# Kernel tuning notes

Hardware: AMD Instinct MI355X
Metric: run time of the kernel (lower is better)

The kernel has to match this reference:

```python
import jax, jax.numpy as jnp
import numpy as np

HIDDEN = 1024
N_HEADS = 16
HEAD_DIM = HIDDEN // N_HEADS  # 64


def setup_inputs() -> dict:
    key = jax.random.key(0)
    k1, k2, k3 = jax.random.split(key, 3)
    x = jax.random.normal(k1, (2, 2048, HIDDEN), dtype=jnp.float32)
    # nn.Linear(hidden, 3*hidden, bias=False): weight [3*hidden, hidden]
    w_qkv = jax.random.normal(k2, (3 * HIDDEN, HIDDEN), dtype=jnp.float32) * (HIDDEN ** -0.5)
    # nn.Linear(hidden, hidden, bias=False): weight [hidden, hidden]
    w_dense = jax.random.normal(k3, (HIDDEN, HIDDEN), dtype=jnp.float32) * (HIDDEN ** -0.5)
    return {"x": x, "w_qkv": w_qkv, "w_dense": w_dense}


def reference(x, w_qkv, w_dense):
    B, S, D = x.shape
    # Fused QKV projection: y = x @ w_qkv.T -> [B, S, 3*D]
    qkv = jnp.einsum("bsd,ed->bse", x, w_qkv)
    q, k, v = jnp.split(qkv, 3, axis=-1)

    def heads(t):  # [B,S,D] -> [B,H,S,hd]
        return t.reshape(B, S, N_HEADS, HEAD_DIM).transpose(0, 2, 1, 3)

    q, k, v = heads(q), heads(k), heads(v)
    scale = jnp.asarray(HEAD_DIM, x.dtype) ** -0.5
    scores = jnp.einsum("bhqd,bhkd->bhqk", q, k) * scale  # [B,H,S,S]
    probs = jax.nn.softmax(scores, axis=-1)
    ctx = jnp.einsum("bhqk,bhkd->bhqd", probs, v)  # [B,H,S,hd]
    ctx = ctx.transpose(0, 2, 1, 3).reshape(B, S, D)
    # Output dense: ctx @ w_dense.T
    return jnp.einsum("bsd,ed->bse", ctx, w_dense)
```

## Files before the change

kernel.cpp:

```cpp
#include <hip/hip_runtime.h>

typedef unsigned short u16;
typedef unsigned int u32;
typedef __bf16 bf16x8 __attribute__((ext_vector_type(8)));
typedef float f32x4 __attribute__((ext_vector_type(4)));
typedef u16 u16x8 __attribute__((ext_vector_type(8)));
typedef u16 u16x4 __attribute__((ext_vector_type(4)));
typedef u32 u32x2 __attribute__((ext_vector_type(2)));

__device__ __forceinline__ u16 to_bf16(float f) {
  unsigned int u = __builtin_bit_cast(unsigned int, f);
  u += 0x7fffu + ((u >> 16) & 1u);
  return (u16)(u >> 16);
}

__device__ __forceinline__ f32x4 mfma16(bf16x8 a, bf16x8 b, f32x4 c) {
  return __builtin_amdgcn_mfma_f32_16x16x32_bf16(a, b, c, 0, 0, 0);
}

#define GLD16(gp, lp) __builtin_amdgcn_global_load_lds( \
    (const __attribute__((address_space(1))) unsigned int*)(gp), \
    (__attribute__((address_space(3))) unsigned int*)(lp), 16, 0, 0)

#define WAITVM(N) asm volatile("s_waitcnt vmcnt(" #N ")" ::: "memory")
#define BARRIER() asm volatile("s_barrier" ::: "memory")

__global__ __launch_bounds__(256) void cvt_all(
    const float* __restrict__ x, const float* __restrict__ wq, const float* __restrict__ wd,
    u16* __restrict__ xb, u16* __restrict__ wqb, u16* __restrict__ wdb) {
  long i = ((long)blockIdx.x * 256 + threadIdx.x) * 4;
  const float* s; u16* d;
  if (i < 4194304)      { s = x  + i;             d = xb  + i; }
  else if (i < 7340032) { s = wq + (i - 4194304); d = wqb + (i - 4194304); }
  else                  { s = wd + (i - 7340032); d = wdb + (i - 7340032); }
  f32x4 f = *(const f32x4*)s;
  u16x4 o;
  o[0] = to_bf16(f[0]); o[1] = to_bf16(f[1]); o[2] = to_bf16(f[2]); o[3] = to_bf16(f[3]);
  *(u16x4*)d = o;
}

__global__ __launch_bounds__(256) void gemm_qkv(const u16* __restrict__ A,
    const u16* __restrict__ Bt, u16* __restrict__ qk, u16* __restrict__ vt,
    int K, float qscale) {
  __shared__ __align__(16) u16 As[2][4096];
  __shared__ __align__(16) u16 Bs[2][4096];
  const int tid = threadIdx.x;
  const int lane = tid & 63, wave = tid >> 6;
  const int wm = (wave & 1) * 64, wn = (wave >> 1) * 64;
  const int bm = blockIdx.y * 128, bn = blockIdx.x * 128;
  const int fm = lane & 15, fk8 = (lane >> 4) * 8;
  f32x4 acc[4][4] = {};

  const int r0 = tid >> 2, c0 = (tid & 3) * 8;
  const u16* Ag = A + (long)(bm + r0) * K + c0;
  const u16* Bg = Bt + (long)(bn + r0) * K + c0;
  const long rowStep = (long)64 * K;

#define GSTAGE(K0, IB) do { \
    GLD16(Ag + (K0),           &As[IB][tid * 8]); \
    GLD16(Ag + rowStep + (K0), &As[IB][tid * 8 + 2048]); \
    GLD16(Bg + (K0),           &Bs[IB][tid * 8]); \
    GLD16(Bg + rowStep + (K0), &Bs[IB][tid * 8 + 2048]); \
  } while (0)

  GSTAGE(0, 0);
  int ib = 0;
  for (int k0 = 0; k0 < K; k0 += 32) {
    if (k0 + 32 < K) { GSTAGE(k0 + 32, ib ^ 1); WAITVM(4); }
    else             { WAITVM(0); }
    BARRIER();
    bf16x8 a[4], b[4];
#pragma unroll
    for (int i = 0; i < 4; i++) a[i] = *(const bf16x8*)&As[ib][(wm + i * 16 + fm) * 32 + fk8];
#pragma unroll
    for (int j = 0; j < 4; j++) b[j] = *(const bf16x8*)&Bs[ib][(wn + j * 16 + fm) * 32 + fk8];
#pragma unroll
    for (int i = 0; i < 4; i++)
#pragma unroll
      for (int j = 0; j < 4; j++)
        acc[i][j] = mfma16(a[i], b[j], acc[i][j]);
    BARRIER();
    ib ^= 1;
  }
#undef GSTAGE

  const int er = (lane >> 4) * 4, ec = lane & 15;
  if (bn >= 2048) {
#pragma unroll
    for (int i = 0; i < 4; i++) {
      const long row0 = bm + wm + i * 16 + er;
      const long bb = row0 >> 11;
      const int kv = (int)(row0 & 2047);
#pragma unroll
      for (int j = 0; j < 4; j++) {
        const int dcol = bn + wn + j * 16 + ec - 2048;
        u16x4 pk;
#pragma unroll
        for (int r = 0; r < 4; r++) pk[r] = to_bf16(acc[i][j][r]);
        *(u16x4*)&vt[((bb * 16 + (dcol >> 6)) * 64 + (dcol & 63)) * 2048 + kv] = pk;
      }
    }
  } else {
    const float sc = (bn < 1024) ? qscale : 1.0f;
#pragma unroll
    for (int i = 0; i < 4; i++)
#pragma unroll
      for (int j = 0; j < 4; j++)
#pragma unroll
        for (int r = 0; r < 4; r++) {
          long row = bm + wm + i * 16 + er + r;
          long col = bn + wn + j * 16 + ec;
          qk[row * 2048 + col] = to_bf16(acc[i][j][r] * sc);
        }
  }
}

__global__ __launch_bounds__(256) void gemm_bt_n64(const u16* __restrict__ A,
    const u16* __restrict__ Bt, float* __restrict__ C, int M, int N, int K) {
  __shared__ __align__(16) u16 As[2][4096];
  __shared__ __align__(16) u16 Bs[2][2048];
  const int tid = threadIdx.x;
  const int lane = tid & 63, wave = tid >> 6;
  const int wm = (wave & 1) * 64, wn = (wave >> 1) * 32;
  const int bm = blockIdx.y * 128, bn = blockIdx.x * 64;
  const int fm = lane & 15, fk8 = (lane >> 4) * 8;
  f32x4 acc[4][2] = {};

  const int r0 = tid >> 2, c0 = (tid & 3) * 8;
  const u16* Ag = A + (long)(bm + r0) * K + c0;
  const u16* Bg = Bt + (long)(bn + r0) * K + c0;
  const long rowStep = (long)64 * K;

#define GSTAGE(K0, IB) do { \
    GLD16(Ag + (K0),           &As[IB][tid * 8]); \
    GLD16(Ag + rowStep + (K0), &As[IB][tid * 8 + 2048]); \
    GLD16(Bg + (K0),           &Bs[IB][tid * 8]); \
  } while (0)

  GSTAGE(0, 0);
  int ib = 0;
  for (int k0 = 0; k0 < K; k0 += 32) {
    if (k0 + 32 < K) { GSTAGE(k0 + 32, ib ^ 1); WAITVM(3); }
    else             { WAITVM(0); }
    BARRIER();
    bf16x8 a[4], b[2];
#pragma unroll
    for (int i = 0; i < 4; i++) a[i] = *(const bf16x8*)&As[ib][(wm + i * 16 + fm) * 32 + fk8];
#pragma unroll
    for (int j = 0; j < 2; j++) b[j] = *(const bf16x8*)&Bs[ib][(wn + j * 16 + fm) * 32 + fk8];
#pragma unroll
    for (int i = 0; i < 4; i++)
#pragma unroll
      for (int j = 0; j < 2; j++)
        acc[i][j] = mfma16(a[i], b[j], acc[i][j]);
    BARRIER();
    ib ^= 1;
  }
#undef GSTAGE

  const int er = (lane >> 4) * 4, ec = lane & 15;
#pragma unroll
  for (int i = 0; i < 4; i++)
#pragma unroll
    for (int j = 0; j < 2; j++)
#pragma unroll
      for (int r = 0; r < 4; r++)
        C[(long)(bm + wm + i * 16 + er + r) * N + bn + wn + j * 16 + ec] = acc[i][j][r];
}

__global__ __launch_bounds__(256) void attn_kernel(const u16* __restrict__ qk,
                                                   const u16* __restrict__ vt,
                                                   u16* __restrict__ ctx) {
  __shared__ __align__(16) u16 Kb[2][4096];
  __shared__ __align__(16) u16 Vb[2][4096];
  __shared__ __align__(16) u16 Ps[128 * 64];
  const int tid = threadIdx.x, lane = tid & 63, wave = tid >> 6;
  const int fm = lane & 15, g = lane >> 4, f7 = fm & 7;

  const int id = blockIdx.x;
  const int c = id & 7, m = id >> 3;
  const int qt = m & 15, bh = (m >> 4) * 8 + c;
  const int b = bh >> 4, h = bh & 15;
  const long tokBase = (long)b * 2048;
  const int q0 = qt * 128;

  const int sr8 = lane >> 3;
  const int gch = (lane & 7) ^ sr8;
  const u16* Kg = qk + (tokBase + wave * 16 + sr8) * 2048 + 1024 + h * 64 + gch * 8;
  const u16* Vg = vt + ((long)bh * 64 + wave * 16 + sr8) * 2048 + gch * 8;
  u16* KL = &Kb[0][wave * 16 * 64] + lane * 8;
  u16* VL = &Vb[0][wave * 16 * 64] + lane * 8;

#define STAGE(S0, IB) do { \
    GLD16(Kg + (long)(S0) * 2048,          KL + (IB) * 4096); \
    GLD16(Kg + (long)((S0) + 8) * 2048,    KL + (IB) * 4096 + 512); \
    GLD16(Vg + (S0),                       VL + (IB) * 4096); \
    GLD16(Vg + (S0) + (long)8 * 2048,      VL + (IB) * 4096 + 512); \
  } while (0)

  STAGE(0, 0);

  bf16x8 qa[2][2];
#pragma unroll
  for (int t = 0; t < 2; t++) {
    const long qoff = (tokBase + q0 + wave * 32 + t * 16 + fm) * 2048 + h * 64;
    qa[t][0] = *(const bf16x8*)&qk[qoff + g * 8];
    qa[t][1] = *(const bf16x8*)&qk[qoff + 32 + g * 8];
  }

  f32x4 o[2][4] = {};
  f32x4 ol[2] = {};
  u16x8 onesu = {0x3F80, 0x3F80, 0x3F80, 0x3F80, 0x3F80, 0x3F80, 0x3F80, 0x3F80};
  bf16x8 ones = __builtin_bit_cast(bf16x8, onesu);

  int ib = 0;
  for (int s0 = 0; s0 < 2048; s0 += 64) {
    if (s0 + 64 < 2048) { STAGE(s0 + 64, ib ^ 1); WAITVM(4); }
    else                { WAITVM(0); }
    BARRIER();

    const u16* Kt = &Kb[ib][0];
    const u16* Vtile = &Vb[ib][0];

#pragma unroll
    for (int jj = 0; jj < 4; jj++) {
      bf16x8 k0 = *(const bf16x8*)&Kt[(jj * 16 + fm) * 64 + ((g    ) ^ f7) * 8];
      bf16x8 k1 = *(const bf16x8*)&Kt[(jj * 16 + fm) * 64 + ((4 + g) ^ f7) * 8];
#pragma unroll
      for (int t = 0; t < 2; t++) {
        f32x4 s = {};
        s = mfma16(k0, qa[t][0], s);
        s = mfma16(k1, qa[t][1], s);
        u32 p0r = __builtin_bit_cast(u32, __builtin_amdgcn_exp2f(s[0])) + 0x8000u;
        u32 p1r = __builtin_bit_cast(u32, __builtin_amdgcn_exp2f(s[1])) + 0x8000u;
        u32 p2r = __builtin_bit_cast(u32, __builtin_amdgcn_exp2f(s[2])) + 0x8000u;
        u32 p3r = __builtin_bit_cast(u32, __builtin_amdgcn_exp2f(s[3])) + 0x8000u;
        u32x2 wv;
        wv[0] = __builtin_amdgcn_perm(p1r, p0r, 0x07060302u);
        wv[1] = __builtin_amdgcn_perm(p3r, p2r, 0x07060302u);
        const int slot = (jj * 4 + g) ^ (2 * f7);
        *(u32x2*)((u32*)&Ps[(wave * 32 + t * 16 + fm) * 64] + slot * 2) = wv;
      }
    }

#pragma unroll
    for (int ks = 0; ks < 2; ks++) {
      bf16x8 vb[4];
#pragma unroll
      for (int jd = 0; jd < 4; jd++)
        vb[jd] = *(const bf16x8*)&Vtile[(jd * 16 + fm) * 64 + ((ks * 4 + g) ^ f7) * 8];
#pragma unroll
      for (int t = 0; t < 2; t++) {
        bf16x8 pa = *(const bf16x8*)&Ps[(wave * 32 + t * 16 + fm) * 64 +
                                        ((4 * ks + g) ^ f7) * 8];
#pragma unroll
        for (int jd = 0; jd < 4; jd++)
          o[t][jd] = mfma16(pa, vb[jd], o[t][jd]);
        ol[t] = mfma16(pa, ones, ol[t]);
      }
    }
    BARRIER();
    ib ^= 1;
  }
#undef STAGE

#pragma unroll
  for (int t = 0; t < 2; t++) {
#pragma unroll
    for (int r = 0; r < 4; r++) {
      float inv = 1.0f / ol[t][r];
      const long obase = (tokBase + q0 + wave * 32 + t * 16 + g * 4 + r) * 1024 + h * 64;
#pragma unroll
      for (int jd = 0; jd < 4; jd++)
        ctx[obase + jd * 16 + fm] = to_bf16(o[t][jd][r] * inv);
    }
  }
}

extern "C" void kernel_launch(void* const* d_in, const int* in_sizes, int n_in,
                              void* d_out, int out_size, void* d_ws, size_t ws_size,
                              hipStream_t stream) {
  const float* x  = (const float*)d_in[0];
  const float* wq = (const float*)d_in[1];
  const float* wd = (const float*)d_in[2];
  float* out = (float*)d_out;
  char* ws = (char*)d_ws;
  u16* xb   = (u16*)(ws);
  u16* wqb  = (u16*)(ws + 8388608);
  u16* wdb  = (u16*)(ws + 14680064);
  u16* qkb  = (u16*)(ws + 16777216);
  u16* vtb  = (u16*)(ws + 33554432);
  u16* ctxb = (u16*)(ws + 41943040);

  const float sscale = 0.125f * 1.44269504f;

  cvt_all<<<8192, 256, 0, stream>>>(x, wq, wd, xb, wqb, wdb);
  gemm_qkv<<<dim3(24, 32), 256, 0, stream>>>(xb, wqb, qkb, vtb, 1024, sscale);
  attn_kernel<<<512, 256, 0, stream>>>(qkb, vtb, ctxb);
  gemm_bt_n64<<<dim3(16, 32), 256, 0, stream>>>(ctxb, wdb, out, 4096, 1024, 1024);
}
```

Before: 180.2 us.

## Split attention KV tile across 8 waves with register-resident P and cross-wave reduction

Attention blocks now use 512 threads. Each of the 8 waves handles 64 queries against a 16-key slice of each 64-key tile, instead of 32 queries against all keys. The probabilities stay in registers as operands for the 16x16x16 bf16 MFMA (packed with v_cvt_pk_bf16_f32), which removes the LDS round-trip for the P matrix. Partial O and row-sum accumulators are merged across the four KV-slice waves through shared memory at the end, and s_setprio is raised around the PV MFMAs. The trade-off is extra reduction barriers, more accumulator registers per wave, and use of the narrower-K MFMA for PV.

```diff
diff --git a/kernel.cpp b/kernel.cpp
--- a/kernel.cpp
+++ b/kernel.cpp
@@ -6,6 +6,7 @@
 typedef float f32x4 __attribute__((ext_vector_type(4)));
 typedef u16 u16x8 __attribute__((ext_vector_type(8)));
 typedef u16 u16x4 __attribute__((ext_vector_type(4)));
+typedef short s16x4 __attribute__((ext_vector_type(4)));
 typedef u32 u32x2 __attribute__((ext_vector_type(2)));
 
 __device__ __forceinline__ u16 to_bf16(float f) {
@@ -16,6 +17,14 @@
 
 __device__ __forceinline__ f32x4 mfma16(bf16x8 a, bf16x8 b, f32x4 c) {
   return __builtin_amdgcn_mfma_f32_16x16x32_bf16(a, b, c, 0, 0, 0);
+}
+
+__device__ __forceinline__ f32x4 mfma1k(s16x4 a, s16x4 b, f32x4 c) {
+  return __builtin_amdgcn_mfma_f32_16x16x16bf16_1k(a, b, c, 0, 0, 0);
+}
+
+__device__ __forceinline__ u32 cvtpk(float a, float b) {
+  u32 r; asm("v_cvt_pk_bf16_f32 %0, %1, %2" : "=v"(r) : "v"(a), "v"(b)); return r;
 }
 
 #define GLD16(gp, lp) __builtin_amdgcn_global_load_lds( \
@@ -168,14 +177,14 @@
         C[(long)(bm + wm + i * 16 + er + r) * N + bn + wn + j * 16 + ec] = acc[i][j][r];
 }
 
-__global__ __launch_bounds__(256) void attn_kernel(const u16* __restrict__ qk,
+__global__ __launch_bounds__(512) void attn_kernel(const u16* __restrict__ qk,
                                                    const u16* __restrict__ vt,
                                                    u16* __restrict__ ctx) {
-  __shared__ __align__(16) u16 Kb[2][4096];
-  __shared__ __align__(16) u16 Vb[2][4096];
-  __shared__ __align__(16) u16 Ps[128 * 64];
+  __shared__ __align__(16) u16 smem[16384];
+  __shared__ __align__(16) float lred[8][64];
   const int tid = threadIdx.x, lane = tid & 63, wave = tid >> 6;
   const int fm = lane & 15, g = lane >> 4, f7 = fm & 7;
+  const int qh = wave & 1, kvq = wave >> 1;
 
   const int id = blockIdx.x;
   const int c = id & 7, m = id >> 3;
@@ -186,93 +195,120 @@
 
   const int sr8 = lane >> 3;
   const int gch = (lane & 7) ^ sr8;
-  const u16* Kg = qk + (tokBase + wave * 16 + sr8) * 2048 + 1024 + h * 64 + gch * 8;
-  const u16* Vg = vt + ((long)bh * 64 + wave * 16 + sr8) * 2048 + gch * 8;
-  u16* KL = &Kb[0][wave * 16 * 64] + lane * 8;
-  u16* VL = &Vb[0][wave * 16 * 64] + lane * 8;
+  const u16* Kg = qk + (tokBase + wave * 8 + sr8) * 2048 + 1024 + h * 64 + gch * 8;
+  const u16* Vg = vt + ((long)bh * 64 + wave * 8 + sr8) * 2048 + gch * 8;
+  u16* KL = &smem[wave * 512] + lane * 8;
+  u16* VL = &smem[8192 + wave * 512] + lane * 8;
 
 #define STAGE(S0, IB) do { \
-    GLD16(Kg + (long)(S0) * 2048,          KL + (IB) * 4096); \
-    GLD16(Kg + (long)((S0) + 8) * 2048,    KL + (IB) * 4096 + 512); \
-    GLD16(Vg + (S0),                       VL + (IB) * 4096); \
-    GLD16(Vg + (S0) + (long)8 * 2048,      VL + (IB) * 4096 + 512); \
+    GLD16(Kg + (long)(S0) * 2048, KL + (IB) * 4096); \
+    GLD16(Vg + (S0),              VL + (IB) * 4096); \
   } while (0)
 
   STAGE(0, 0);
 
-  bf16x8 qa[2][2];
-#pragma unroll
-  for (int t = 0; t < 2; t++) {
-    const long qoff = (tokBase + q0 + wave * 32 + t * 16 + fm) * 2048 + h * 64;
-    qa[t][0] = *(const bf16x8*)&qk[qoff + g * 8];
-    qa[t][1] = *(const bf16x8*)&qk[qoff + 32 + g * 8];
-  }
-
-  f32x4 o[2][4] = {};
-  f32x4 ol[2] = {};
-  u16x8 onesu = {0x3F80, 0x3F80, 0x3F80, 0x3F80, 0x3F80, 0x3F80, 0x3F80, 0x3F80};
-  bf16x8 ones = __builtin_bit_cast(bf16x8, onesu);
+  bf16x8 qa[4][2];
+#pragma unroll
+  for (int qb = 0; qb < 4; qb++) {
+    const long qoff = (tokBase + q0 + qh * 64 + qb * 16 + fm) * 2048 + h * 64;
+    qa[qb][0] = *(const bf16x8*)&qk[qoff + g * 8];
+    qa[qb][1] = *(const bf16x8*)&qk[qoff + 32 + g * 8];
+  }
+
+  f32x4 o[4][4] = {};
+  f32x4 ol[4] = {};
+  const s16x4 onesb = {0x3F80, 0x3F80, 0x3F80, 0x3F80};
 
   int ib = 0;
   for (int s0 = 0; s0 < 2048; s0 += 64) {
-    if (s0 + 64 < 2048) { STAGE(s0 + 64, ib ^ 1); WAITVM(4); }
+    if (s0 + 64 < 2048) { STAGE(s0 + 64, ib ^ 1); WAITVM(2); }
     else                { WAITVM(0); }
     BARRIER();
-
-    const u16* Kt = &Kb[ib][0];
-    const u16* Vtile = &Vb[ib][0];
-
-#pragma unroll
-    for (int jj = 0; jj < 4; jj++) {
-      bf16x8 k0 = *(const bf16x8*)&Kt[(jj * 16 + fm) * 64 + ((g    ) ^ f7) * 8];
-      bf16x8 k1 = *(const bf16x8*)&Kt[(jj * 16 + fm) * 64 + ((4 + g) ^ f7) * 8];
-#pragma unroll
-      for (int t = 0; t < 2; t++) {
-        f32x4 s = {};
-        s = mfma16(k0, qa[t][0], s);
-        s = mfma16(k1, qa[t][1], s);
-        u32 p0r = __builtin_bit_cast(u32, __builtin_amdgcn_exp2f(s[0])) + 0x8000u;
-        u32 p1r = __builtin_bit_cast(u32, __builtin_amdgcn_exp2f(s[1])) + 0x8000u;
-        u32 p2r = __builtin_bit_cast(u32, __builtin_amdgcn_exp2f(s[2])) + 0x8000u;
-        u32 p3r = __builtin_bit_cast(u32, __builtin_amdgcn_exp2f(s[3])) + 0x8000u;
-        u32x2 wv;
-        wv[0] = __builtin_amdgcn_perm(p1r, p0r, 0x07060302u);
-        wv[1] = __builtin_amdgcn_perm(p3r, p2r, 0x07060302u);
-        const int slot = (jj * 4 + g) ^ (2 * f7);
-        *(u32x2*)((u32*)&Ps[(wave * 32 + t * 16 + fm) * 64] + slot * 2) = wv;
-      }
+    const u16* Kt = &smem[ib * 4096];
+    const u16* Vt = &smem[8192 + ib * 4096];
+
+    bf16x8 ka0 = *(const bf16x8*)&Kt[(kvq * 16 + fm) * 64 + ((g) ^ f7) * 8];
+    bf16x8 ka1 = *(const bf16x8*)&Kt[(kvq * 16 + fm) * 64 + ((4 + g) ^ f7) * 8];
+    u16x4 vbu[4];
+#pragma unroll
+    for (int db = 0; db < 4; db++)
+      vbu[db] = *(const u16x4*)&Vt[(db * 16 + fm) * 64 +
+                                   ((kvq * 2 + (g >> 1)) ^ f7) * 8 + (g & 1) * 4];
+
+    s16x4 pa[4];
+#pragma unroll
+    for (int qb = 0; qb < 4; qb++) {
+      f32x4 s = {};
+      s = mfma16(ka0, qa[qb][0], s);
+      s = mfma16(ka1, qa[qb][1], s);
+      u32x2 pk;
+      pk[0] = cvtpk(__builtin_amdgcn_exp2f(s[0]), __builtin_amdgcn_exp2f(s[1]));
+      pk[1] = cvtpk(__builtin_amdgcn_exp2f(s[2]), __builtin_amdgcn_exp2f(s[3]));
+      pa[qb] = __builtin_bit_cast(s16x4, pk);
     }
 
-#pragma unroll
-    for (int ks = 0; ks < 2; ks++) {
-      bf16x8 vb[4];
-#pragma unroll
-      for (int jd = 0; jd < 4; jd++)
-        vb[jd] = *(const bf16x8*)&Vtile[(jd * 16 + fm) * 64 + ((ks * 4 + g) ^ f7) * 8];
-#pragma unroll
-      for (int t = 0; t < 2; t++) {
-        bf16x8 pa = *(const bf16x8*)&Ps[(wave * 32 + t * 16 + fm) * 64 +
-                                        ((4 * ks + g) ^ f7) * 8];
-#pragma unroll
-        for (int jd = 0; jd < 4; jd++)
-          o[t][jd] = mfma16(pa, vb[jd], o[t][jd]);
-        ol[t] = mfma16(pa, ones, ol[t]);
-      }
+    __builtin_amdgcn_s_setprio(1);
+#pragma unroll
+    for (int qb = 0; qb < 4; qb++) {
+#pragma unroll
+      for (int db = 0; db < 4; db++)
+        o[qb][db] = mfma1k(pa[qb], __builtin_bit_cast(s16x4, vbu[db]), o[qb][db]);
+      ol[qb] = mfma1k(pa[qb], onesb, ol[qb]);
     }
+    __builtin_amdgcn_s_setprio(0);
     BARRIER();
     ib ^= 1;
   }
 #undef STAGE
 
-#pragma unroll
-  for (int t = 0; t < 2; t++) {
-#pragma unroll
-    for (int r = 0; r < 4; r++) {
-      float inv = 1.0f / ol[t][r];
-      const long obase = (tokBase + q0 + wave * 32 + t * 16 + g * 4 + r) * 1024 + h * 64;
-#pragma unroll
-      for (int jd = 0; jd < 4; jd++)
-        ctx[obase + jd * 16 + fm] = to_bf16(o[t][jd][r] * inv);
+  __syncthreads();
+  float* red = (float*)&smem[0];
+
+#define WR_O(SLOT) do { \
+    _Pragma("unroll") for (int qb = 0; qb < 4; qb++) { \
+      _Pragma("unroll") for (int db = 0; db < 4; db++) \
+        *(f32x4*)&red[(SLOT) * 4096 + (qb * 4 + db) * 256 + lane * 4] = o[qb][db]; \
+      if (fm == 0) *(f32x4*)&lred[wave][qb * 16 + g * 4] = ol[qb]; \
+    } \
+  } while (0)
+
+#define RD_O(SLOT, PW) do { \
+    _Pragma("unroll") for (int qb = 0; qb < 4; qb++) { \
+      _Pragma("unroll") for (int db = 0; db < 4; db++) { \
+        f32x4 t = *(const f32x4*)&red[(SLOT) * 4096 + (qb * 4 + db) * 256 + lane * 4]; \
+        o[qb][db] += t; \
+      } \
+      f32x4 lt = *(const f32x4*)&lred[PW][qb * 16 + g * 4]; \
+      ol[qb] += lt; \
+    } \
+  } while (0)
+
+  if (wave == 4 || wave == 5) WR_O(wave - 4);
+  __syncthreads();
+  if (wave == 0 || wave == 1) RD_O(wave, wave + 4);
+  __syncthreads();
+  if (wave == 6 || wave == 7) WR_O(wave - 6);
+  __syncthreads();
+  if (wave == 2 || wave == 3) RD_O(wave - 2, wave + 4);
+  __syncthreads();
+  if (wave == 2 || wave == 3) WR_O(wave - 2);
+  __syncthreads();
+  if (wave == 0 || wave == 1) RD_O(wave, wave + 2);
+#undef WR_O
+#undef RD_O
+
+  if (wave < 2) {
+#pragma unroll
+    for (int qb = 0; qb < 4; qb++) {
+      f32x4 inv;
+#pragma unroll
+      for (int r = 0; r < 4; r++) inv[r] = 1.0f / ol[qb][r];
+#pragma unroll
+      for (int db = 0; db < 4; db++)
+#pragma unroll
+        for (int r = 0; r < 4; r++)
+          ctx[(tokBase + q0 + qh * 64 + qb * 16 + g * 4 + r) * 1024 + h * 64 + db * 16 + fm] =
+              to_bf16(o[qb][db][r] * inv[r]);
     }
   }
 }
@@ -296,6 +332,6 @@
 
   cvt_all<<<8192, 256, 0, stream>>>(x, wq, wd, xb, wqb, wdb);
   gemm_qkv<<<dim3(24, 32), 256, 0, stream>>>(xb, wqb, qkb, vtb, 1024, sscale);
-  attn_kernel<<<512, 256, 0, stream>>>(qkb, vtb, ctxb);
+  attn_kernel<<<512, 512, 0, stream>>>(qkb, vtb, ctxb);
   gemm_bt_n64<<<dim3(16, 32), 256, 0, stream>>>(ctxb, wdb, out, 4096, 1024, 1024);
 }
```

After: 209.0 us. 1.16x slower.
